# Kernel tuning notes

Measured on AMD Instinct MI355X. Metric: run time of the kernel, lower is better.

Reference implementation:

```python
import jax, jax.numpy as jnp
import numpy as np

NEG_INF = float(np.finfo(np.float32).min)


def setup_inputs() -> dict:
    key = jax.random.key(0)
    k1, k2, k3 = jax.random.split(key, 3)
    n_context, d_model = 4096, 2048
    x = jax.random.normal(k1, (n_context, d_model), dtype=jnp.float32)
    # nn.Linear default init scale ~ 1/sqrt(fan_in); use small weights for numeric sanity
    W_qk = jax.random.normal(k2, (d_model, d_model), dtype=jnp.float32) / np.sqrt(d_model)
    W_ov = jax.random.normal(k3, (d_model, d_model), dtype=jnp.float32) / np.sqrt(d_model)
    return {"x": x, "W_qk": W_qk, "W_ov": W_ov}


def reference(x, W_qk, W_ov):
    # Faithful to: softmax(X @ W_qk.T @ X.T + causal_mask) @ X @ W_ov.T
    # (biases of the torch Linears are never used in forward)
    n = x.shape[0]
    q = x @ W_qk.T                      # [n, d]
    scores = q @ x.T                    # [n, n]  (no 1/sqrt(d) scaling, as in source)
    causal = jnp.tril(jnp.ones((n, n), dtype=bool))
    scores = jnp.where(causal, scores, NEG_INF)  # additive -inf mask equivalent
    attn = jax.nn.softmax(scores, axis=-1)       # [n, n]
    out = (attn @ x) @ W_ov.T                    # [n, d]
    return out
```

## Files before the change

### kernel.cpp

```cpp
#include <hip/hip_runtime.h>
#include <hip/hip_bf16.h>
#include <stdint.h>
#include <stddef.h>
#include <math.h>

typedef _Float16 f16;
typedef __attribute__((ext_vector_type(8))) _Float16 f16x8;
typedef __attribute__((ext_vector_type(4))) float    f32x4;

constexpr int BM = 128, BN = 128, BK = 64;

#define GLOAD_LDS16(gp, lp)                                        \
    __builtin_amdgcn_global_load_lds(                              \
        (const __attribute__((address_space(1))) unsigned int*)(gp),\
        (__attribute__((address_space(3))) unsigned int*)(lp), 16, 0, 0)

#define MFMA_TILE(AV, BV)                                                     \
    do {                                                                      \
        __builtin_amdgcn_s_setprio(1);                                        \
        _Pragma("unroll")                                                     \
        for (int mi_ = 0; mi_ < 4; ++mi_)                                     \
            _Pragma("unroll")                                                 \
            for (int ni_ = 0; ni_ < 4; ++ni_)                                 \
                acc[mi_][ni_] = __builtin_amdgcn_mfma_f32_16x16x32_f16(       \
                    (AV)[mi_], (BV)[ni_], acc[mi_][ni_], 0, 0, 0);            \
        __builtin_amdgcn_s_setprio(0);                                        \
    } while (0)

template <int EPI>
__global__ __launch_bounds__(512, 2) void gemm8_a2(
    const f16* __restrict__ Ah, const f16* __restrict__ Al,
    const f16* __restrict__ B,
    float* __restrict__ Cf, f16* __restrict__ Co, f16* __restrict__ Clo,
    int M, int N, int K)
{
    const int bx = blockIdx.x;
    const int by = blockIdx.y;

    const int tid   = threadIdx.x;
    const int lane  = tid & 63;
    const int wave  = tid >> 6;
    const int wm    = wave >> 2;
    const int wn    = wave & 3;
    const int lrow  = lane & 15;
    const int lquad = lane >> 4;

    __shared__ f16 lds[2][32768];

    const int row0 = by * 128;
    const int col0 = bx * 256;

    const int srow = tid >> 3;
    const int scol = ((tid & 7) ^ (srow & 7)) * 8;
    const int loff = wave * 512;

    const int g0 = ((lquad)     ^ (lrow & 7)) * 8;
    const int g1 = ((4 + lquad) ^ (lrow & 7)) * 8;

    const int arow = (wm * 64 + lrow) * 64;
    const int brow = (wn * 64 + lrow) * 64 + 16384;

    const f16* gAh = Ah + (size_t)(row0 + srow) * K + scol;
    const f16* gAl = Al + (size_t)(row0 + srow) * K + scol;
    const f16* gB  = B  + (size_t)(col0 + srow) * K + scol;
    const size_t r64 = (size_t)64 * K;

    f32x4 acc[4][4];
    const f32x4 fz = {0.f, 0.f, 0.f, 0.f};
    #pragma unroll
    for (int i = 0; i < 4; ++i)
        #pragma unroll
        for (int j = 0; j < 4; ++j) acc[i][j] = fz;

    const int nt = K / 64;

    #pragma unroll
    for (int u = 0; u < 4; ++u)
        GLOAD_LDS16(gB + u * r64, &lds[0][16384 + u * 4096 + loff]);
    #pragma unroll
    for (int u = 0; u < 2; ++u)
        GLOAD_LDS16(gAh + u * r64, &lds[0][u * 4096 + loff]);
    #pragma unroll
    for (int u = 0; u < 2; ++u)
        GLOAD_LDS16(gAl + u * r64, &lds[0][8192 + u * 4096 + loff]);
    asm volatile("s_waitcnt vmcnt(2)");
    __builtin_amdgcn_s_barrier();

    auto tile_body = [&](int t, bool stage) {
        const int cur = t & 1;
        const size_t kn = (size_t)(t + 1) * 64;
        const f16* bufc = &lds[cur][0];
        f16* bufn = &lds[cur ^ 1][0];

        f16x8 av[4], bv0[4], bv1[4];

        #pragma unroll
        for (int mi = 0; mi < 4; ++mi)
            av[mi] = *(const f16x8*)&bufc[arow + mi * 1024 + g0];
        #pragma unroll
        for (int ni = 0; ni < 4; ++ni)
            bv0[ni] = *(const f16x8*)&bufc[brow + ni * 1024 + g0];
        if (stage) {
            GLOAD_LDS16(gB + kn,       &bufn[16384 + loff]);
            GLOAD_LDS16(gB + r64 + kn, &bufn[16384 + 4096 + loff]);
        }
        __builtin_amdgcn_s_barrier();
        asm volatile("s_waitcnt lgkmcnt(0)");
        MFMA_TILE(av, bv0);
        __builtin_amdgcn_s_barrier();

        #pragma unroll
        for (int mi = 0; mi < 4; ++mi)
            av[mi] = *(const f16x8*)&bufc[arow + mi * 1024 + g1];
        #pragma unroll
        for (int ni = 0; ni < 4; ++ni)
            bv1[ni] = *(const f16x8*)&bufc[brow + ni * 1024 + g1];
        if (stage) {
            GLOAD_LDS16(gB + 2 * r64 + kn, &bufn[16384 +  8192 + loff]);
            GLOAD_LDS16(gB + 3 * r64 + kn, &bufn[16384 + 12288 + loff]);
            asm volatile("s_waitcnt vmcnt(4)");
        } else {
            asm volatile("s_waitcnt vmcnt(0)");
        }
        __builtin_amdgcn_s_barrier();
        asm volatile("s_waitcnt lgkmcnt(0)");
        MFMA_TILE(av, bv1);
        __builtin_amdgcn_s_barrier();

        #pragma unroll
        for (int mi = 0; mi < 4; ++mi)
            av[mi] = *(const f16x8*)&bufc[8192 + arow + mi * 1024 + g0];
        if (stage) {
            GLOAD_LDS16(gAh + kn,       &bufn[loff]);
            GLOAD_LDS16(gAh + r64 + kn, &bufn[4096 + loff]);
        }
        __builtin_amdgcn_s_barrier();
        asm volatile("s_waitcnt lgkmcnt(0)");
        MFMA_TILE(av, bv0);
        __builtin_amdgcn_s_barrier();

        #pragma unroll
        for (int mi = 0; mi < 4; ++mi)
            av[mi] = *(const f16x8*)&bufc[8192 + arow + mi * 1024 + g1];
        if (stage) {
            GLOAD_LDS16(gAl + kn,       &bufn[ 8192 + loff]);
            GLOAD_LDS16(gAl + r64 + kn, &bufn[12288 + loff]);
        }
        asm volatile("s_waitcnt vmcnt(2)");
        __builtin_amdgcn_s_barrier();
        asm volatile("s_waitcnt lgkmcnt(0)");
        MFMA_TILE(av, bv1);
        __builtin_amdgcn_s_barrier();
    };

    for (int t = 0; t < nt - 1; ++t) tile_body(t, true);
    tile_body(nt - 1, false);

    #pragma unroll
    for (int mi = 0; mi < 4; ++mi) {
        #pragma unroll
        for (int ni = 0; ni < 4; ++ni) {
            #pragma unroll
            for (int r = 0; r < 4; ++r) {
                const int row = row0 + wm * 64 + mi * 16 + lquad * 4 + r;
                const int col = col0 + wn * 64 + ni * 16 + lrow;
                const size_t idx = (size_t)row * N + col;
                const float v = acc[mi][ni][r];
                if (EPI == 0) {
                    Cf[idx] = v;
                } else {
                    const f16 h = (f16)v;
                    Co[idx]  = h;
                    Clo[idx] = (f16)(v - (float)h);
                }
            }
        }
    }
}

__global__ __launch_bounds__(512, 2) void gemm8_s_jobs(
    const f16* __restrict__ Ah, const f16* __restrict__ Al,
    const f16* __restrict__ B,
    float* __restrict__ Cf, int N, int K)
{
    const int b = blockIdx.x;
    const int j = (b & 7) * 32 + (b >> 3);
    int r = (int)sqrtf((float)j);
    while (r * r > j) --r;
    while ((r + 1) * (r + 1) <= j) ++r;
    const int u = j - r * r;
    const int by = (u < r) ? 2 * r : 2 * r + 1;
    const int bx = (u < r) ? u : u - r;

    const int tid   = threadIdx.x;
    const int lane  = tid & 63;
    const int wave  = tid >> 6;
    const int wm    = wave >> 2;
    const int wn    = wave & 3;
    const int lrow  = lane & 15;
    const int lquad = lane >> 4;

    __shared__ f16 lds[2][32768];

    const int row0 = by * 128;
    const int col0 = bx * 256;

    const int srow = tid >> 3;
    const int scol = ((tid & 7) ^ (srow & 7)) * 8;
    const int loff = wave * 512;

    const int g0 = ((lquad)     ^ (lrow & 7)) * 8;
    const int g1 = ((4 + lquad) ^ (lrow & 7)) * 8;

    const int arow = (wm * 64 + lrow) * 64;
    const int brow = (wn * 64 + lrow) * 64 + 16384;

    const f16* gAh = Ah + (size_t)(row0 + srow) * K + scol;
    const f16* gAl = Al + (size_t)(row0 + srow) * K + scol;
    const f16* gB  = B  + (size_t)(col0 + srow) * K + scol;
    const size_t r64 = (size_t)64 * K;

    f32x4 acc[4][4];
    const f32x4 fz = {0.f, 0.f, 0.f, 0.f};
    #pragma unroll
    for (int i = 0; i < 4; ++i)
        #pragma unroll
        for (int jj = 0; jj < 4; ++jj) acc[i][jj] = fz;

    const int nt = K / 64;

    #pragma unroll
    for (int u2 = 0; u2 < 4; ++u2)
        GLOAD_LDS16(gB + u2 * r64, &lds[0][16384 + u2 * 4096 + loff]);
    #pragma unroll
    for (int u2 = 0; u2 < 2; ++u2)
        GLOAD_LDS16(gAh + u2 * r64, &lds[0][u2 * 4096 + loff]);
    #pragma unroll
    for (int u2 = 0; u2 < 2; ++u2)
        GLOAD_LDS16(gAl + u2 * r64, &lds[0][8192 + u2 * 4096 + loff]);
    asm volatile("s_waitcnt vmcnt(2)");
    __builtin_amdgcn_s_barrier();

    auto tile_body = [&](int t, bool stage) {
        const int cur = t & 1;
        const size_t kn = (size_t)(t + 1) * 64;
        const f16* bufc = &lds[cur][0];
        f16* bufn = &lds[cur ^ 1][0];

        f16x8 av[4], bv0[4], bv1[4];

        #pragma unroll
        for (int mi = 0; mi < 4; ++mi)
            av[mi] = *(const f16x8*)&bufc[arow + mi * 1024 + g0];
        #pragma unroll
        for (int ni = 0; ni < 4; ++ni)
            bv0[ni] = *(const f16x8*)&bufc[brow + ni * 1024 + g0];
        if (stage) {
            GLOAD_LDS16(gB + kn,       &bufn[16384 + loff]);
            GLOAD_LDS16(gB + r64 + kn, &bufn[16384 + 4096 + loff]);
        }
        __builtin_amdgcn_s_barrier();
        asm volatile("s_waitcnt lgkmcnt(0)");
        MFMA_TILE(av, bv0);
        __builtin_amdgcn_s_barrier();

        #pragma unroll
        for (int mi = 0; mi < 4; ++mi)
            av[mi] = *(const f16x8*)&bufc[arow + mi * 1024 + g1];
        #pragma unroll
        for (int ni = 0; ni < 4; ++ni)
            bv1[ni] = *(const f16x8*)&bufc[brow + ni * 1024 + g1];
        if (stage) {
            GLOAD_LDS16(gB + 2 * r64 + kn, &bufn[16384 +  8192 + loff]);
            GLOAD_LDS16(gB + 3 * r64 + kn, &bufn[16384 + 12288 + loff]);
            asm volatile("s_waitcnt vmcnt(4)");
        } else {
            asm volatile("s_waitcnt vmcnt(0)");
        }
        __builtin_amdgcn_s_barrier();
        asm volatile("s_waitcnt lgkmcnt(0)");
        MFMA_TILE(av, bv1);
        __builtin_amdgcn_s_barrier();

        #pragma unroll
        for (int mi = 0; mi < 4; ++mi)
            av[mi] = *(const f16x8*)&bufc[8192 + arow + mi * 1024 + g0];
        if (stage) {
            GLOAD_LDS16(gAh + kn,       &bufn[loff]);
            GLOAD_LDS16(gAh + r64 + kn, &bufn[4096 + loff]);
        }
        __builtin_amdgcn_s_barrier();
        asm volatile("s_waitcnt lgkmcnt(0)");
        MFMA_TILE(av, bv0);
        __builtin_amdgcn_s_barrier();

        #pragma unroll
        for (int mi = 0; mi < 4; ++mi)
            av[mi] = *(const f16x8*)&bufc[8192 + arow + mi * 1024 + g1];
        if (stage) {
            GLOAD_LDS16(gAl + kn,       &bufn[ 8192 + loff]);
            GLOAD_LDS16(gAl + r64 + kn, &bufn[12288 + loff]);
        }
        asm volatile("s_waitcnt vmcnt(2)");
        __builtin_amdgcn_s_barrier();
        asm volatile("s_waitcnt lgkmcnt(0)");
        MFMA_TILE(av, bv1);
        __builtin_amdgcn_s_barrier();
    };

    for (int t = 0; t < nt - 1; ++t) tile_body(t, true);
    tile_body(nt - 1, false);

    #pragma unroll
    for (int mi = 0; mi < 4; ++mi) {
        #pragma unroll
        for (int ni = 0; ni < 4; ++ni) {
            #pragma unroll
            for (int rr = 0; rr < 4; ++rr) {
                const int row = row0 + wm * 64 + mi * 16 + lquad * 4 + rr;
                const int col = col0 + wn * 64 + ni * 16 + lrow;
                Cf[(size_t)row * N + col] = acc[mi][ni][rr];
            }
        }
    }
}

__global__ __launch_bounds__(256) void gemm_half_splitk(
    const f16* __restrict__ Ah, const f16* __restrict__ Al,
    const f16* __restrict__ B, float* __restrict__ Spart, int Kg)
{
    const int kc = blockIdx.x;
    const int h  = blockIdx.y;
    const int row0 = h * 256;
    const int kbeg = kc * 256;

    const int tid   = threadIdx.x;
    const int lane  = tid & 63;
    const int wave  = tid >> 6;
    const int wm    = wave >> 1;
    const int wn    = wave & 1;
    const int lrow  = lane & 15;
    const int lquad = lane >> 4;

    __shared__ f16 sAh[BM * BK];
    __shared__ f16 sAl[BM * BK];
    __shared__ f16 sB [BM * BK];

    const int srow = tid >> 3;
    const int scol = (((tid & 7) ^ ((tid >> 3) & 7))) * 8;
    const int lbase = wave * 512;

    f32x4 acc[4][4];
    const f32x4 fz = {0.f, 0.f, 0.f, 0.f};
    #pragma unroll
    for (int i = 0; i < 4; ++i)
        #pragma unroll
        for (int jj = 0; jj < 4; ++jj) acc[i][jj] = fz;

    for (int k0 = kbeg; k0 < kbeg + 256; k0 += BK) {
        __syncthreads();
        #pragma unroll
        for (int r = 0; r < 4; ++r) {
            const int trow = srow + 32 * r;
            const size_t ga = (size_t)(row0 + trow) * Kg + k0 + scol;
            const int ldst = lbase + r * 2048;
            GLOAD_LDS16(&Ah[ga], &sAh[ldst]);
            GLOAD_LDS16(&Al[ga], &sAl[ldst]);
            GLOAD_LDS16(&B [ga], &sB [ldst]);
        }
        __syncthreads();

        #pragma unroll
        for (int kk = 0; kk < 2; ++kk) {
            const int grpA = ((kk * 4 + lquad) ^ (lrow & 7)) * 8;
            f16x8 ah[4], al[4], bv[4];
            #pragma unroll
            for (int mi = 0; mi < 4; ++mi) {
                const int off = (wm * 64 + mi * 16 + lrow) * BK + grpA;
                ah[mi] = *reinterpret_cast<const f16x8*>(&sAh[off]);
                al[mi] = *reinterpret_cast<const f16x8*>(&sAl[off]);
            }
            #pragma unroll
            for (int ni = 0; ni < 4; ++ni)
                bv[ni] = *reinterpret_cast<const f16x8*>(
                    &sB[(wn * 64 + ni * 16 + lrow) * BK + grpA]);

            #pragma unroll
            for (int mi = 0; mi < 4; ++mi)
                #pragma unroll
                for (int ni = 0; ni < 4; ++ni) {
                    acc[mi][ni] = __builtin_amdgcn_mfma_f32_16x16x32_f16(
                        ah[mi], bv[ni], acc[mi][ni], 0, 0, 0);
                    acc[mi][ni] = __builtin_amdgcn_mfma_f32_16x16x32_f16(
                        al[mi], bv[ni], acc[mi][ni], 0, 0, 0);
                }
        }
    }

    float* outp = Spart + ((size_t)(kc * 16 + h)) * (128 * 128);
    #pragma unroll
    for (int mi = 0; mi < 4; ++mi) {
        #pragma unroll
        for (int ni = 0; ni < 4; ++ni) {
            #pragma unroll
            for (int r = 0; r < 4; ++r) {
                const int row = wm * 64 + mi * 16 + lquad * 4 + r;
                const int col = wn * 64 + ni * 16 + lrow;
                outp[row * 128 + col] = acc[mi][ni][r];
            }
        }
    }
}

__global__ __launch_bounds__(256) void combine_halves(
    const float* __restrict__ Spart, float* __restrict__ S, int n)
{
    const int h = blockIdx.y;
    const int e = (blockIdx.x * 256 + threadIdx.x) * 4;
    float4 a = *reinterpret_cast<const float4*>(
        &Spart[(size_t)h * (128 * 128) + e]);
    #pragma unroll
    for (int kc = 1; kc < 8; ++kc) {
        const float4 b = *reinterpret_cast<const float4*>(
            &Spart[(size_t)(kc * 16 + h) * (128 * 128) + e]);
        a.x += b.x; a.y += b.y; a.z += b.z; a.w += b.w;
    }
    const int i = e >> 7, jj = e & 127;
    *reinterpret_cast<float4*>(&S[(size_t)(h * 256 + i) * n + h * 256 + jj]) = a;
}

template <int EPI, bool KCAUSAL>
__global__ __launch_bounds__(512, 2) void gemm8_1t(
    const f16* __restrict__ A, const f16* __restrict__ B,
    float* __restrict__ Cf, f16* __restrict__ Co,
    int M, int N, int K)
{
    const int bx = blockIdx.x;
    const int by = KCAUSAL ? ((int)gridDim.y - 1 - (int)blockIdx.y) : blockIdx.y;

    const int tid   = threadIdx.x;
    const int lane  = tid & 63;
    const int wave  = tid >> 6;
    const int wm    = wave >> 2;
    const int wn    = wave & 3;
    const int lrow  = lane & 15;
    const int lquad = lane >> 4;

    __shared__ f16 lds[3][24576];

    const int row0 = by * 128;
    const int col0 = bx * 256;

    const int srow = tid >> 3;
    const int scol = ((tid & 7) ^ (srow & 7)) * 8;
    const int loff = wave * 512;
    const int g0 = ((lquad)     ^ (lrow & 7)) * 8;
    const int g1 = ((4 + lquad) ^ (lrow & 7)) * 8;
    const int arow = (wm * 64 + lrow) * 64;
    const int brow = (wn * 64 + lrow) * 64 + 8192;

    const f16* gA = A + (size_t)(row0 + srow) * K + scol;
    const f16* gB = B + (size_t)(col0 + srow) * K + scol;
    const size_t r64 = (size_t)64 * K;

    f32x4 acc[4][4];
    const f32x4 fz = {0.f, 0.f, 0.f, 0.f};
    #pragma unroll
    for (int i = 0; i < 4; ++i)
        #pragma unroll
        for (int j = 0; j < 4; ++j) acc[i][j] = fz;

    const int Keff = KCAUSAL ? (by + 1) * 128 : K;
    const int nt = Keff / 64;

    #pragma unroll
    for (int tt = 0; tt < 2; ++tt) {
        const size_t kk = (size_t)tt * 64;
        #pragma unroll
        for (int u = 0; u < 4; ++u)
            GLOAD_LDS16(gB + u * r64 + kk, &lds[tt][8192 + u * 4096 + loff]);
        #pragma unroll
        for (int u = 0; u < 2; ++u)
            GLOAD_LDS16(gA + u * r64 + kk, &lds[tt][u * 4096 + loff]);
    }
    asm volatile("s_waitcnt vmcnt(6)");
    __builtin_amdgcn_s_barrier();

    int cur = 0;
    for (int t = 0; t < nt; ++t) {
        const int nb = (cur >= 1) ? (cur - 1) : (cur + 2);
        const bool stage2 = (t + 2 < nt);
        const size_t kn = (size_t)(t + 2) * 64;
        const f16* bufc = &lds[cur][0];
        f16* bufn = &lds[nb][0];

        f16x8 av[4], bv[4];

        #pragma unroll
        for (int mi = 0; mi < 4; ++mi)
            av[mi] = *(const f16x8*)&bufc[arow + mi * 1024 + g0];
        #pragma unroll
        for (int ni = 0; ni < 4; ++ni)
            bv[ni] = *(const f16x8*)&bufc[brow + ni * 1024 + g0];
        if (stage2) {
            GLOAD_LDS16(gB + kn,           &bufn[8192 + loff]);
            GLOAD_LDS16(gB + r64 + kn,     &bufn[8192 + 4096 + loff]);
            GLOAD_LDS16(gB + 2 * r64 + kn, &bufn[8192 + 8192 + loff]);
        }
        __builtin_amdgcn_s_barrier();
        asm volatile("s_waitcnt lgkmcnt(0)");
        MFMA_TILE(av, bv);
        __builtin_amdgcn_s_barrier();

        #pragma unroll
        for (int mi = 0; mi < 4; ++mi)
            av[mi] = *(const f16x8*)&bufc[arow + mi * 1024 + g1];
        #pragma unroll
        for (int ni = 0; ni < 4; ++ni)
            bv[ni] = *(const f16x8*)&bufc[brow + ni * 1024 + g1];
        if (stage2) {
            GLOAD_LDS16(gB + 3 * r64 + kn, &bufn[8192 + 12288 + loff]);
            GLOAD_LDS16(gA + kn,           &bufn[loff]);
            GLOAD_LDS16(gA + r64 + kn,     &bufn[4096 + loff]);
            asm volatile("s_waitcnt vmcnt(6)");
        } else {
            asm volatile("s_waitcnt vmcnt(0)");
        }
        __builtin_amdgcn_s_barrier();
        asm volatile("s_waitcnt lgkmcnt(0)");
        MFMA_TILE(av, bv);
        __builtin_amdgcn_s_barrier();

        cur = (cur == 2) ? 0 : cur + 1;
    }

    #pragma unroll
    for (int mi = 0; mi < 4; ++mi) {
        #pragma unroll
        for (int ni = 0; ni < 4; ++ni) {
            #pragma unroll
            for (int r = 0; r < 4; ++r) {
                const int row = row0 + wm * 64 + mi * 16 + lquad * 4 + r;
                const int col = col0 + wn * 64 + ni * 16 + lrow;
                const size_t idx = (size_t)row * N + col;
                const float v = acc[mi][ni][r];
                if (EPI == 0) Cf[idx] = v;
                else          Co[idx] = (f16)v;
            }
        }
    }
}

__global__ __launch_bounds__(256) void split_f32_f16(
    const float* __restrict__ in, f16* __restrict__ hi, f16* __restrict__ lo,
    size_t nelem)
{
    const size_t i = ((size_t)blockIdx.x * 256 + threadIdx.x) * 4;
    if (i >= nelem) return;
    const float4 v = *reinterpret_cast<const float4*>(in + i);
    union { f16 h[4]; ushort4 u; } H, L;
    H.h[0] = (f16)v.x; H.h[1] = (f16)v.y; H.h[2] = (f16)v.z; H.h[3] = (f16)v.w;
    *reinterpret_cast<ushort4*>(hi + i) = H.u;
    if (lo) {
        L.h[0] = (f16)(v.x - (float)H.h[0]);
        L.h[1] = (f16)(v.y - (float)H.h[1]);
        L.h[2] = (f16)(v.z - (float)H.h[2]);
        L.h[3] = (f16)(v.w - (float)H.h[3]);
        *reinterpret_cast<ushort4*>(lo + i) = L.u;
    }
}

__global__ __launch_bounds__(256) void prep_x(
    const float* __restrict__ in, f16* __restrict__ hi, f16* __restrict__ lo,
    f16* __restrict__ tr, int rows, int cols)
{
    __shared__ float tile[32][33];
    const int bx = blockIdx.x;
    const int by = blockIdx.y;
    const int tx = threadIdx.x & 31;
    const int ty = threadIdx.x >> 5;
    #pragma unroll
    for (int r = 0; r < 4; ++r) {
        const int row = by * 32 + ty + 8 * r;
        const int col = bx * 32 + tx;
        const float v = in[(size_t)row * cols + col];
        tile[ty + 8 * r][tx] = v;
        const f16 h = (f16)v;
        hi[(size_t)row * cols + col] = h;
        lo[(size_t)row * cols + col] = (f16)(v - (float)h);
    }
    __syncthreads();
    #pragma unroll
    for (int r = 0; r < 4; ++r)
        tr[(size_t)(bx * 32 + ty + 8 * r) * rows + by * 32 + tx] =
            (f16)tile[tx][ty + 8 * r];
}

__global__ __launch_bounds__(256) void softmax_rows(
    const float* __restrict__ S, f16* __restrict__ P, int n)
{
    const int row = blockIdx.x;
    const int len = row + 1;
    const int padlen = ((row >> 7) + 1) << 7;
    const float* srow = S + (size_t)row * n;
    f16* prow = P + (size_t)row * n;
    const int tid = threadIdx.x;
    const int lane = tid & 63, wave = tid >> 6;
    __shared__ float rowbuf[4096];
    __shared__ float redm[4], reds[4];

    float m = -3.0e38f, s = 0.f;
    for (int j = tid; j < len; j += 256) {
        const float v = srow[j];
        rowbuf[j] = v;
        const float mn = fmaxf(m, v);
        s = s * __expf(m - mn) + __expf(v - mn);
        m = mn;
    }
    #pragma unroll
    for (int off = 32; off; off >>= 1) {
        const float mo = __shfl_xor(m, off, 64);
        const float so = __shfl_xor(s, off, 64);
        const float mn = fmaxf(m, mo);
        s = s * __expf(m - mn) + so * __expf(mo - mn);
        m = mn;
    }
    if (lane == 0) { redm[wave] = m; reds[wave] = s; }
    __syncthreads();
    float M = redm[0], Sm = reds[0];
    #pragma unroll
    for (int w = 1; w < 4; ++w) {
        const float mn = fmaxf(M, redm[w]);
        Sm = Sm * __expf(M - mn) + reds[w] * __expf(redm[w] - mn);
        M = mn;
    }
    const float inv = 1.0f / Sm;

    const f16 z = (f16)0.0f;
    for (int j = tid; j < padlen; j += 256)
        prow[j] = (j < len) ? (f16)(__expf(rowbuf[j] - M) * inv) : z;
}

extern "C" void kernel_launch(void* const* d_in, const int* in_sizes, int n_in,
                              void* d_out, int out_size, void* d_ws, size_t ws_size,
                              hipStream_t stream)
{
    const int n = 4096, d = 2048;
    const float* x   = (const float*)d_in[0];
    const float* Wqk = (const float*)d_in[1];
    const float* Wov = (const float*)d_in[2];
    float* out = (float*)d_out;

    char* ws = (char*)d_ws;
    const size_t MB = 1 << 20;
    f16*   xh   = (f16*)  (ws);
    f16*   xl   = (f16*)  (ws + 16 * MB);
    f16*   Wh   = (f16*)  (ws + 32 * MB);
    f16*   Wovh = (f16*)  (ws + 40 * MB);
    f16*   xTh  = (f16*)  (ws + 48 * MB);
    f16*   qh   = (f16*)  (ws + 64 * MB);
    f16*   ql   = (f16*)  (ws + 80 * MB);
    float* S    = (float*)(ws + 96 * MB);
    float* Sp   = (float*)(ws + 16 * MB);
    f16*   P    = (f16*)  (ws);
    f16*   o    = (f16*)  (ws + 64 * MB);

    const dim3 blk(256);
    const dim3 blk8(512);

    split_f32_f16<<<dim3((d * d) / (256 * 4)), blk, 0, stream>>>(Wqk, Wh, nullptr, (size_t)d * d);
    split_f32_f16<<<dim3((d * d) / (256 * 4)), blk, 0, stream>>>(Wov, Wovh, nullptr, (size_t)d * d);
    prep_x<<<dim3(d / 32, n / 32), blk, 0, stream>>>(x, xh, xl, xTh, n, d);

    gemm8_a2<1><<<dim3(d / 256, n / 128), blk8, 0, stream>>>(
        xh, xl, Wh, nullptr, qh, ql, n, d, d);

    gemm8_s_jobs<<<dim3(256), blk8, 0, stream>>>(qh, ql, xh, S, n, d);
    gemm_half_splitk<<<dim3(8, 16), blk, 0, stream>>>(qh, ql, xh, Sp, d);
    combine_halves<<<dim3(16, 16), blk, 0, stream>>>(Sp, S, n);

    softmax_rows<<<dim3(n), blk, 0, stream>>>(S, P, n);

    gemm8_1t<2, true><<<dim3(d / 256, n / 128), blk8, 0, stream>>>(
        P, xTh, nullptr, o, n, d, n);

    gemm8_1t<0, false><<<dim3(d / 256, n / 128), blk8, 0, stream>>>(
        o, Wovh, out, nullptr, n, d, d);
}
```

Measured before the change: 380.4 us.

## Collapse per-tile barriers: batch LDS fragment reads then issue all MFMAs

Rewrites the main loops of the split-fp16 and half GEMM kernels so each K tile reads all A/B fragments from LDS at once, issues all next-tile global->LDS loads together, then runs the MFMAs back-to-back with a single wait and barrier at the end. This removes several workgroup barriers and lgkmcnt waits per tile. In exchange it raises register pressure with more live fragment vectors. The double-buffered kernels now wait for all outstanding global loads every tile, which may expose more memory latency.

```diff
diff --git a/kernel.cpp b/kernel.cpp
--- a/kernel.cpp
+++ b/kernel.cpp
@@ -83,78 +83,55 @@
     #pragma unroll
     for (int u = 0; u < 2; ++u)
         GLOAD_LDS16(gAl + u * r64, &lds[0][8192 + u * 4096 + loff]);
-    asm volatile("s_waitcnt vmcnt(2)");
+    asm volatile("s_waitcnt vmcnt(0)");
     __builtin_amdgcn_s_barrier();
 
-    auto tile_body = [&](int t, bool stage) {
-        const int cur = t & 1;
+    for (int t = 0; t < nt; ++t) {
+        const f16* bufc = &lds[t & 1][0];
+        f16* bufn = &lds[(t + 1) & 1][0];
+        const bool stage = (t + 1 < nt);
         const size_t kn = (size_t)(t + 1) * 64;
-        const f16* bufc = &lds[cur][0];
-        f16* bufn = &lds[cur ^ 1][0];
-
-        f16x8 av[4], bv0[4], bv1[4];
-
-        #pragma unroll
-        for (int mi = 0; mi < 4; ++mi)
-            av[mi] = *(const f16x8*)&bufc[arow + mi * 1024 + g0];
+
+        f16x8 ah0[4], ah1[4], al0[4], al1[4], bv0[4], bv1[4];
+
+        #pragma unroll
+        for (int mi = 0; mi < 4; ++mi)
+            ah0[mi] = *(const f16x8*)&bufc[arow + mi * 1024 + g0];
         #pragma unroll
         for (int ni = 0; ni < 4; ++ni)
             bv0[ni] = *(const f16x8*)&bufc[brow + ni * 1024 + g0];
-        if (stage) {
-            GLOAD_LDS16(gB + kn,       &bufn[16384 + loff]);
-            GLOAD_LDS16(gB + r64 + kn, &bufn[16384 + 4096 + loff]);
-        }
-        __builtin_amdgcn_s_barrier();
-        asm volatile("s_waitcnt lgkmcnt(0)");
-        MFMA_TILE(av, bv0);
-        __builtin_amdgcn_s_barrier();
-
-        #pragma unroll
-        for (int mi = 0; mi < 4; ++mi)
-            av[mi] = *(const f16x8*)&bufc[arow + mi * 1024 + g1];
+        #pragma unroll
+        for (int mi = 0; mi < 4; ++mi)
+            ah1[mi] = *(const f16x8*)&bufc[arow + mi * 1024 + g1];
         #pragma unroll
         for (int ni = 0; ni < 4; ++ni)
             bv1[ni] = *(const f16x8*)&bufc[brow + ni * 1024 + g1];
+        #pragma unroll
+        for (int mi = 0; mi < 4; ++mi)
+            al0[mi] = *(const f16x8*)&bufc[8192 + arow + mi * 1024 + g0];
+        #pragma unroll
+        for (int mi = 0; mi < 4; ++mi)
+            al1[mi] = *(const f16x8*)&bufc[8192 + arow + mi * 1024 + g1];
+
         if (stage) {
+            GLOAD_LDS16(gB + kn,           &bufn[16384 + loff]);
+            GLOAD_LDS16(gB + r64 + kn,     &bufn[16384 +  4096 + loff]);
             GLOAD_LDS16(gB + 2 * r64 + kn, &bufn[16384 +  8192 + loff]);
             GLOAD_LDS16(gB + 3 * r64 + kn, &bufn[16384 + 12288 + loff]);
-            asm volatile("s_waitcnt vmcnt(4)");
-        } else {
-            asm volatile("s_waitcnt vmcnt(0)");
-        }
+            GLOAD_LDS16(gAh + kn,          &bufn[loff]);
+            GLOAD_LDS16(gAh + r64 + kn,    &bufn[4096 + loff]);
+            GLOAD_LDS16(gAl + kn,          &bufn[ 8192 + loff]);
+            GLOAD_LDS16(gAl + r64 + kn,    &bufn[12288 + loff]);
+        }
+
+        MFMA_TILE(ah0, bv0);
+        MFMA_TILE(ah1, bv1);
+        MFMA_TILE(al0, bv0);
+        MFMA_TILE(al1, bv1);
+
+        asm volatile("s_waitcnt vmcnt(0)");
         __builtin_amdgcn_s_barrier();
-        asm volatile("s_waitcnt lgkmcnt(0)");
-        MFMA_TILE(av, bv1);
-        __builtin_amdgcn_s_barrier();
-
-        #pragma unroll
-        for (int mi = 0; mi < 4; ++mi)
-            av[mi] = *(const f16x8*)&bufc[8192 + arow + mi * 1024 + g0];
-        if (stage) {
-            GLOAD_LDS16(gAh + kn,       &bufn[loff]);
-            GLOAD_LDS16(gAh + r64 + kn, &bufn[4096 + loff]);
-        }
-        __builtin_amdgcn_s_barrier();
-        asm volatile("s_waitcnt lgkmcnt(0)");
-        MFMA_TILE(av, bv0);
-        __builtin_amdgcn_s_barrier();
-
-        #pragma unroll
-        for (int mi = 0; mi < 4; ++mi)
-            av[mi] = *(const f16x8*)&bufc[8192 + arow + mi * 1024 + g1];
-        if (stage) {
-            GLOAD_LDS16(gAl + kn,       &bufn[ 8192 + loff]);
-            GLOAD_LDS16(gAl + r64 + kn, &bufn[12288 + loff]);
-        }
-        asm volatile("s_waitcnt vmcnt(2)");
-        __builtin_amdgcn_s_barrier();
-        asm volatile("s_waitcnt lgkmcnt(0)");
-        MFMA_TILE(av, bv1);
-        __builtin_amdgcn_s_barrier();
-    };
-
-    for (int t = 0; t < nt - 1; ++t) tile_body(t, true);
-    tile_body(nt - 1, false);
+    }
 
     #pragma unroll
     for (int mi = 0; mi < 4; ++mi) {
@@ -238,78 +215,55 @@
     #pragma unroll
     for (int u2 = 0; u2 < 2; ++u2)
         GLOAD_LDS16(gAl + u2 * r64, &lds[0][8192 + u2 * 4096 + loff]);
-    asm volatile("s_waitcnt vmcnt(2)");
+    asm volatile("s_waitcnt vmcnt(0)");
     __builtin_amdgcn_s_barrier();
 
-    auto tile_body = [&](int t, bool stage) {
-        const int cur = t & 1;
+    for (int t = 0; t < nt; ++t) {
+        const f16* bufc = &lds[t & 1][0];
+        f16* bufn = &lds[(t + 1) & 1][0];
+        const bool stage = (t + 1 < nt);
         const size_t kn = (size_t)(t + 1) * 64;
-        const f16* bufc = &lds[cur][0];
-        f16* bufn = &lds[cur ^ 1][0];
-
-        f16x8 av[4], bv0[4], bv1[4];
-
-        #pragma unroll
-        for (int mi = 0; mi < 4; ++mi)
-            av[mi] = *(const f16x8*)&bufc[arow + mi * 1024 + g0];
+
+        f16x8 ah0[4], ah1[4], al0[4], al1[4], bv0[4], bv1[4];
+
+        #pragma unroll
+        for (int mi = 0; mi < 4; ++mi)
+            ah0[mi] = *(const f16x8*)&bufc[arow + mi * 1024 + g0];
         #pragma unroll
         for (int ni = 0; ni < 4; ++ni)
             bv0[ni] = *(const f16x8*)&bufc[brow + ni * 1024 + g0];
-        if (stage) {
-            GLOAD_LDS16(gB + kn,       &bufn[16384 + loff]);
-            GLOAD_LDS16(gB + r64 + kn, &bufn[16384 + 4096 + loff]);
-        }
-        __builtin_amdgcn_s_barrier();
-        asm volatile("s_waitcnt lgkmcnt(0)");
-        MFMA_TILE(av, bv0);
-        __builtin_amdgcn_s_barrier();
-
-        #pragma unroll
-        for (int mi = 0; mi < 4; ++mi)
-            av[mi] = *(const f16x8*)&bufc[arow + mi * 1024 + g1];
+        #pragma unroll
+        for (int mi = 0; mi < 4; ++mi)
+            ah1[mi] = *(const f16x8*)&bufc[arow + mi * 1024 + g1];
         #pragma unroll
         for (int ni = 0; ni < 4; ++ni)
             bv1[ni] = *(const f16x8*)&bufc[brow + ni * 1024 + g1];
+        #pragma unroll
+        for (int mi = 0; mi < 4; ++mi)
+            al0[mi] = *(const f16x8*)&bufc[8192 + arow + mi * 1024 + g0];
+        #pragma unroll
+        for (int mi = 0; mi < 4; ++mi)
+            al1[mi] = *(const f16x8*)&bufc[8192 + arow + mi * 1024 + g1];
+
         if (stage) {
+            GLOAD_LDS16(gB + kn,           &bufn[16384 + loff]);
+            GLOAD_LDS16(gB + r64 + kn,     &bufn[16384 +  4096 + loff]);
             GLOAD_LDS16(gB + 2 * r64 + kn, &bufn[16384 +  8192 + loff]);
             GLOAD_LDS16(gB + 3 * r64 + kn, &bufn[16384 + 12288 + loff]);
-            asm volatile("s_waitcnt vmcnt(4)");
-        } else {
-            asm volatile("s_waitcnt vmcnt(0)");
-        }
+            GLOAD_LDS16(gAh + kn,          &bufn[loff]);
+            GLOAD_LDS16(gAh + r64 + kn,    &bufn[4096 + loff]);
+            GLOAD_LDS16(gAl + kn,          &bufn[ 8192 + loff]);
+            GLOAD_LDS16(gAl + r64 + kn,    &bufn[12288 + loff]);
+        }
+
+        MFMA_TILE(ah0, bv0);
+        MFMA_TILE(ah1, bv1);
+        MFMA_TILE(al0, bv0);
+        MFMA_TILE(al1, bv1);
+
+        asm volatile("s_waitcnt vmcnt(0)");
         __builtin_amdgcn_s_barrier();
-        asm volatile("s_waitcnt lgkmcnt(0)");
-        MFMA_TILE(av, bv1);
-        __builtin_amdgcn_s_barrier();
-
-        #pragma unroll
-        for (int mi = 0; mi < 4; ++mi)
-            av[mi] = *(const f16x8*)&bufc[8192 + arow + mi * 1024 + g0];
-        if (stage) {
-            GLOAD_LDS16(gAh + kn,       &bufn[loff]);
-            GLOAD_LDS16(gAh + r64 + kn, &bufn[4096 + loff]);
-        }
-        __builtin_amdgcn_s_barrier();
-        asm volatile("s_waitcnt lgkmcnt(0)");
-        MFMA_TILE(av, bv0);
-        __builtin_amdgcn_s_barrier();
-
-        #pragma unroll
-        for (int mi = 0; mi < 4; ++mi)
-            av[mi] = *(const f16x8*)&bufc[8192 + arow + mi * 1024 + g1];
-        if (stage) {
-            GLOAD_LDS16(gAl + kn,       &bufn[ 8192 + loff]);
-            GLOAD_LDS16(gAl + r64 + kn, &bufn[12288 + loff]);
-        }
-        asm volatile("s_waitcnt vmcnt(2)");
-        __builtin_amdgcn_s_barrier();
-        asm volatile("s_waitcnt lgkmcnt(0)");
-        MFMA_TILE(av, bv1);
-        __builtin_amdgcn_s_barrier();
-    };
-
-    for (int t = 0; t < nt - 1; ++t) tile_body(t, true);
-    tile_body(nt - 1, false);
+    }
 
     #pragma unroll
     for (int mi = 0; mi < 4; ++mi) {
@@ -494,41 +448,35 @@
         const f16* bufc = &lds[cur][0];
         f16* bufn = &lds[nb][0];
 
-        f16x8 av[4], bv[4];
-
-        #pragma unroll
-        for (int mi = 0; mi < 4; ++mi)
-            av[mi] = *(const f16x8*)&bufc[arow + mi * 1024 + g0];
+        f16x8 av0[4], av1[4], bv0[4], bv1[4];
+
+        #pragma unroll
+        for (int mi = 0; mi < 4; ++mi)
+            av0[mi] = *(const f16x8*)&bufc[arow + mi * 1024 + g0];
         #pragma unroll
         for (int ni = 0; ni < 4; ++ni)
-            bv[ni] = *(const f16x8*)&bufc[brow + ni * 1024 + g0];
+            bv0[ni] = *(const f16x8*)&bufc[brow + ni * 1024 + g0];
+        #pragma unroll
+        for (int mi = 0; mi < 4; ++mi)
+            av1[mi] = *(const f16x8*)&bufc[arow + mi * 1024 + g1];
+        #pragma unroll
+        for (int ni = 0; ni < 4; ++ni)
+            bv1[ni] = *(const f16x8*)&bufc[brow + ni * 1024 + g1];
+
         if (stage2) {
             GLOAD_LDS16(gB + kn,           &bufn[8192 + loff]);
-            GLOAD_LDS16(gB + r64 + kn,     &bufn[8192 + 4096 + loff]);
-            GLOAD_LDS16(gB + 2 * r64 + kn, &bufn[8192 + 8192 + loff]);
-        }
-        __builtin_amdgcn_s_barrier();
-        asm volatile("s_waitcnt lgkmcnt(0)");
-        MFMA_TILE(av, bv);
-        __builtin_amdgcn_s_barrier();
-
-        #pragma unroll
-        for (int mi = 0; mi < 4; ++mi)
-            av[mi] = *(const f16x8*)&bufc[arow + mi * 1024 + g1];
-        #pragma unroll
-        for (int ni = 0; ni < 4; ++ni)
-            bv[ni] = *(const f16x8*)&bufc[brow + ni * 1024 + g1];
-        if (stage2) {
+            GLOAD_LDS16(gB + r64 + kn,     &bufn[8192 +  4096 + loff]);
+            GLOAD_LDS16(gB + 2 * r64 + kn, &bufn[8192 +  8192 + loff]);
             GLOAD_LDS16(gB + 3 * r64 + kn, &bufn[8192 + 12288 + loff]);
             GLOAD_LDS16(gA + kn,           &bufn[loff]);
             GLOAD_LDS16(gA + r64 + kn,     &bufn[4096 + loff]);
-            asm volatile("s_waitcnt vmcnt(6)");
-        } else {
-            asm volatile("s_waitcnt vmcnt(0)");
-        }
-        __builtin_amdgcn_s_barrier();
-        asm volatile("s_waitcnt lgkmcnt(0)");
-        MFMA_TILE(av, bv);
+        }
+
+        MFMA_TILE(av0, bv0);
+        MFMA_TILE(av1, bv1);
+
+        if (stage2) asm volatile("s_waitcnt vmcnt(6)");
+        else        asm volatile("s_waitcnt vmcnt(0)");
         __builtin_amdgcn_s_barrier();
 
         cur = (cur == 2) ? 0 : cur + 1;
```

Result: faster. 365.9 us (-3.8%).
